# Kernel tuning notes

Hardware: AMD Instinct MI355X
Metric: run time of the kernel (lower is better)

The kernel has to match this reference:

```python
import jax, jax.numpy as jnp
import numpy as np

N = 100000
E = 3200000
D_IN = 128
D_OUT = 64


def setup_inputs() -> dict:
    key = jax.random.key(0)
    k1, k2, k3 = jax.random.split(key, 3)
    x = jax.random.normal(k1, (N, D_IN), dtype=jnp.float32)
    edge_index = jax.random.randint(k2, (2, E), 0, N, dtype=jnp.int64)
    # Glorot-ish init for the GCN weight, zero bias (PyG default has bias)
    W = jax.random.normal(k3, (D_IN, D_OUT), dtype=jnp.float32) * (1.0 / np.sqrt(D_IN))
    b = jnp.zeros((D_OUT,), dtype=jnp.float32)
    return {"x": x, "edge_index": edge_index, "W": W, "b": b}


def gcn_conv(x, edge_index, W, b):
    # PyG GCNConv: add self-loops, symmetric degree normalization,
    # linear transform, then normalized scatter-add aggregation.
    n = x.shape[0]
    self_loops = jnp.arange(n, dtype=edge_index.dtype)
    row = jnp.concatenate([edge_index[0], self_loops])  # targets
    col = jnp.concatenate([edge_index[1], self_loops])  # sources

    ones = jnp.ones_like(row, dtype=x.dtype)
    deg = jax.ops.segment_sum(ones, row, num_segments=n)  # [N]
    deg_inv_sqrt = jnp.where(deg > 0, jax.lax.rsqrt(deg), 0.0)
    norm = deg_inv_sqrt[row] * deg_inv_sqrt[col]  # [E+N]

    h = x @ W  # [N, d_out] -- transform before aggregation (cheap GEMM)
    msgs = norm[:, None] * h[col]  # gather + scale: [E+N, d_out]
    out = jax.ops.segment_sum(msgs, row, num_segments=n)  # scatter-add
    return out + b


def reference(x, edge_index, W, b):
    # CRD.forward: relu(GCNConv(x, edge_index)); dropout is identity in eval.
    return jax.nn.relu(gcn_conv(x, edge_index, W, b))
```

## Files before the change

kernel.cpp:

```cpp
#include <hip/hip_runtime.h>

#define D_IN 128
#define D_OUT 64
#define RSH 7
#define RPS 128
#define NS 1024
#define ACH 5120
#define AREG 10
#define PREG 25
#define CSHIFT 17
#define CMASK 0x1FFFFu

typedef unsigned int u32;
typedef __attribute__((ext_vector_type(8))) short bf16x8;
typedef __attribute__((ext_vector_type(4))) float f32x4;

__device__ inline float u2f(u32 u) {
    union { u32 i; float f; } v; v.i = u; return v.f;
}
__device__ inline unsigned short f2bf(float f) {
    union { float f; u32 i; } v; v.f = f;
    u32 r = v.i + 0x7fffu + ((v.i >> 16) & 1u);
    return (unsigned short)(r >> 16);
}

__global__ __launch_bounds__(256) void k_hist(
    const int* __restrict__ row, u32* __restrict__ stot, int E) {
    __shared__ u32 cnt[NS];
    for (int t = threadIdx.x; t < NS; t += 256) cnt[t] = 0;
    __syncthreads();
    const int stride = gridDim.x * 256;
    for (int e = blockIdx.x * 256 + threadIdx.x; e < E; e += stride)
        atomicAdd(&cnt[(u32)__builtin_nontemporal_load(&row[e]) >> RSH], 1u);
    __syncthreads();
    for (int t = threadIdx.x; t < NS; t += 256) {
        u32 c = cnt[t];
        if (c) atomicAdd(&stot[t], c);
    }
}

__global__ __launch_bounds__(1024) void k_scan1024(
    const u32* __restrict__ stot, u32* __restrict__ sstart,
    u32* __restrict__ gcur, int E) {
    __shared__ u32 tmp[1024];
    const int t = threadIdx.x;
    u32 v = stot[t];
    tmp[t] = v;
    __syncthreads();
    for (int off = 1; off < 1024; off <<= 1) {
        u32 u = (t >= off) ? tmp[t - off] : 0;
        __syncthreads();
        tmp[t] += u;
        __syncthreads();
    }
    u32 ex = tmp[t] - v;
    sstart[t] = ex;
    gcur[t] = ex;
    if (t == 1023) sstart[1024] = (u32)E;
}

__global__ __launch_bounds__(512) void k_part(
    const int* __restrict__ row, const int* __restrict__ col,
    u32* __restrict__ gcur, u32* __restrict__ pk, int E, int CH) {
    __shared__ u32 cnt[NS];
    const int lo = blockIdx.x * CH, hi = min(E, lo + CH);
    const int tid = threadIdx.x;
    u32 rw[PREG], cw[PREG];
#pragma unroll
    for (int k = 0; k < PREG; ++k) {
        int e = lo + tid + k * 512;
        if (e < hi) {
            rw[k] = (u32)__builtin_nontemporal_load(&row[e]);
            cw[k] = (u32)__builtin_nontemporal_load(&col[e]);
        }
    }
    for (int t = tid; t < NS; t += 512) cnt[t] = 0;
    __syncthreads();
#pragma unroll
    for (int k = 0; k < PREG; ++k)
        if (lo + tid + k * 512 < hi) atomicAdd(&cnt[rw[k] >> RSH], 1u);
    __syncthreads();
    for (int t = tid; t < NS; t += 512) {
        u32 c = cnt[t];
        cnt[t] = c ? atomicAdd(&gcur[t], c) : 0u;
    }
    __syncthreads();
#pragma unroll
    for (int k = 0; k < PREG; ++k)
        if (lo + tid + k * 512 < hi) {
            u32 pos = atomicAdd(&cnt[rw[k] >> RSH], 1u);
            pk[pos] = ((rw[k] & (RPS - 1u)) << CSHIFT) | cw[k];
        }
}

__global__ __launch_bounds__(256) void k_deg(
    const u32* __restrict__ pk, const u32* __restrict__ sstart,
    float* __restrict__ dinv, int n) {
    __shared__ u32 cnt[RPS];
    const int s = blockIdx.x, lo = s << RSH;
    if (threadIdx.x < RPS) cnt[threadIdx.x] = 0;
    __syncthreads();
    const u32 beg = sstart[s], end = sstart[s + 1];
    for (u32 i = beg + threadIdx.x; i < end; i += 256)
        atomicAdd(&cnt[pk[i] >> CSHIFT], 1u);
    __syncthreads();
    for (int t = threadIdx.x; t < RPS && lo + t < n; t += 256)
        dinv[lo + t] = rsqrtf((float)(cnt[t] + 1u));
}

__global__ __launch_bounds__(256, 4) void k_gemm(
    const float* __restrict__ x, const float* __restrict__ W,
    const float* __restrict__ dinv, unsigned short* __restrict__ h, int n) {
    __shared__ float Wl[D_IN * D_OUT];
    for (int idx = threadIdx.x; idx < D_IN * D_OUT; idx += 256)
        Wl[idx] = W[idx];
    __syncthreads();

    const int lane = threadIdx.x & 63;
    const int wave = threadIdx.x >> 6;
    const int m = lane & 15, kg = lane >> 4;

    bf16x8 bfr[4][4];
#pragma unroll
    for (int kb = 0; kb < 4; ++kb)
#pragma unroll
        for (int nb = 0; nb < 4; ++nb) {
            bf16x8 f;
#pragma unroll
            for (int j = 0; j < 8; ++j)
                f[j] = (short)f2bf(Wl[(kb * 32 + kg * 8 + j) * D_OUT + nb * 16 + m]);
            bfr[kb][nb] = f;
        }

    const int ntile = (n + 15) >> 4;
    for (int tile = blockIdx.x * 4 + wave; tile < ntile; tile += gridDim.x * 4) {
        const int i0 = tile << 4;
        const int arow = min(i0 + m, n - 1);
        const float* xr = &x[(size_t)arow * D_IN + kg * 8];

        f32x4 acc[4];
#pragma unroll
        for (int nb = 0; nb < 4; ++nb) acc[nb] = (f32x4){0.f, 0.f, 0.f, 0.f};

#pragma unroll
        for (int kb = 0; kb < 4; ++kb) {
            float4 xa = *(const float4*)(xr + kb * 32);
            float4 xb = *(const float4*)(xr + kb * 32 + 4);
            bf16x8 af;
            af[0] = (short)f2bf(xa.x); af[1] = (short)f2bf(xa.y);
            af[2] = (short)f2bf(xa.z); af[3] = (short)f2bf(xa.w);
            af[4] = (short)f2bf(xb.x); af[5] = (short)f2bf(xb.y);
            af[6] = (short)f2bf(xb.z); af[7] = (short)f2bf(xb.w);
#pragma unroll
            for (int nb = 0; nb < 4; ++nb)
                acc[nb] = __builtin_amdgcn_mfma_f32_16x16x32_bf16(
                    af, bfr[kb][nb], acc[nb], 0, 0, 0);
        }
#pragma unroll
        for (int i = 0; i < 4; ++i) {
            int r = i0 + kg * 4 + i;
            if (r < n) {
                float d = dinv[r];
#pragma unroll
                for (int nb = 0; nb < 4; ++nb)
                    h[(size_t)r * D_OUT + nb * 16 + m] = f2bf(d * acc[nb][i]);
            }
        }
    }
}

__global__ __launch_bounds__(512, 4) void k_aggr(
    const unsigned short* __restrict__ h, const u32* __restrict__ pk,
    const u32* __restrict__ sstart, const float* __restrict__ dinv,
    const float* __restrict__ bias, float* __restrict__ out, int n) {
    __shared__ u32 cnt[RPS], eptr[RPS], cur[RPS];
    __shared__ u32 cols[ACH];
    const int s = blockIdx.x, lo = s << RSH;
    const int rows = min(RPS, n - lo);
    const int tid = threadIdx.x;
    const int wave = tid >> 6, lane = tid & 63;
    const int qd = lane >> 4, l15 = lane & 15;
    const uint2* hp2 = (const uint2*)h;

    float a0[16], a1[16], a2[16], a3[16];
#pragma unroll
    for (int k = 0; k < 16; ++k) { a0[k] = 0.f; a1[k] = 0.f; a2[k] = 0.f; a3[k] = 0.f; }

    const u32 beg = sstart[s], end = sstart[s + 1];
    for (u32 cb = beg; cb < end; cb += ACH) {
        const u32 ce = min(end, cb + (u32)ACH);
        const int m = (int)(ce - cb);
        u32 w[AREG];
#pragma unroll
        for (int k = 0; k < AREG; ++k) {
            int i = tid + k * 512;
            if (i < m) w[k] = __builtin_nontemporal_load(&pk[cb + i]);
        }
        if (tid < RPS) cnt[tid] = 0;
        __syncthreads();
#pragma unroll
        for (int k = 0; k < AREG; ++k)
            if (tid + k * 512 < m) atomicAdd(&cnt[w[k] >> CSHIFT], 1u);
        __syncthreads();
        if (tid < 64) {
            u32 c0 = cnt[2 * tid], c1 = cnt[2 * tid + 1];
            u32 sv = c0 + c1;
#pragma unroll
            for (int d = 1; d < 64; d <<= 1) {
                u32 t = __shfl_up(sv, d);
                if (tid >= d) sv += t;
            }
            u32 ex = sv - (c0 + c1);
            eptr[2 * tid] = ex;          cur[2 * tid] = ex;
            eptr[2 * tid + 1] = ex + c0; cur[2 * tid + 1] = ex + c0;
        }
        __syncthreads();
#pragma unroll
        for (int k = 0; k < AREG; ++k)
            if (tid + k * 512 < m) {
                u32 pos = atomicAdd(&cur[w[k] >> CSHIFT], 1u);
                cols[pos] = w[k] & CMASK;
            }
        __syncthreads();
#pragma unroll
        for (int k = 0; k < 16; ++k) {
            int q = wave + 8 * k;
            if (q < rows) {
                const int b1 = (int)eptr[q] + (int)cnt[q];
                int t = (int)eptr[q];
                for (; t + 32 <= b1; t += 32) {
                    u32 c[8]; uint2 u[8];
#pragma unroll
                    for (int j = 0; j < 8; ++j) c[j] = cols[t + 4 * j + qd];
#pragma unroll
                    for (int j = 0; j < 8; ++j) u[j] = hp2[(size_t)c[j] * 16 + l15];
#pragma unroll
                    for (int j = 0; j < 8; ++j) {
                        a0[k] += u2f(u[j].x << 16); a1[k] += u2f(u[j].x & 0xffff0000u);
                        a2[k] += u2f(u[j].y << 16); a3[k] += u2f(u[j].y & 0xffff0000u);
                    }
                }
                for (; t + 16 <= b1; t += 16) {
                    u32 c[4]; uint2 u[4];
#pragma unroll
                    for (int j = 0; j < 4; ++j) c[j] = cols[t + 4 * j + qd];
#pragma unroll
                    for (int j = 0; j < 4; ++j) u[j] = hp2[(size_t)c[j] * 16 + l15];
#pragma unroll
                    for (int j = 0; j < 4; ++j) {
                        a0[k] += u2f(u[j].x << 16); a1[k] += u2f(u[j].x & 0xffff0000u);
                        a2[k] += u2f(u[j].y << 16); a3[k] += u2f(u[j].y & 0xffff0000u);
                    }
                }
                for (; t + 4 <= b1; t += 4) {
                    u32 c = cols[t + qd];
                    uint2 u = hp2[(size_t)c * 16 + l15];
                    a0[k] += u2f(u.x << 16); a1[k] += u2f(u.x & 0xffff0000u);
                    a2[k] += u2f(u.y << 16); a3[k] += u2f(u.y & 0xffff0000u);
                }
                const int rem = b1 - t;
                if (qd < rem) {
                    u32 c = cols[t + qd];
                    uint2 u = hp2[(size_t)c * 16 + l15];
                    a0[k] += u2f(u.x << 16); a1[k] += u2f(u.x & 0xffff0000u);
                    a2[k] += u2f(u.y << 16); a3[k] += u2f(u.y & 0xffff0000u);
                }
            }
        }
        __syncthreads();
    }
#pragma unroll
    for (int k = 0; k < 16; ++k) {
        int q = wave + 8 * k;
        if (q >= rows) continue;
        float r0 = a0[k], r1 = a1[k], r2 = a2[k], r3 = a3[k];
        r0 += __shfl_xor(r0, 16); r0 += __shfl_xor(r0, 32);
        r1 += __shfl_xor(r1, 16); r1 += __shfl_xor(r1, 32);
        r2 += __shfl_xor(r2, 16); r2 += __shfl_xor(r2, 32);
        r3 += __shfl_xor(r3, 16); r3 += __shfl_xor(r3, 32);
        int i = lo + q;
        uint2 us = hp2[(size_t)i * 16 + l15];
        r0 += u2f(us.x << 16); r1 += u2f(us.x & 0xffff0000u);
        r2 += u2f(us.y << 16); r3 += u2f(us.y & 0xffff0000u);
        float d = dinv[i];
        float4 bb = *(const float4*)&bias[l15 * 4];
        float4 o;
        o.x = fmaxf(fmaf(d, r0, bb.x), 0.f);
        o.y = fmaxf(fmaf(d, r1, bb.y), 0.f);
        o.z = fmaxf(fmaf(d, r2, bb.z), 0.f);
        o.w = fmaxf(fmaf(d, r3, bb.w), 0.f);
        if (qd == 0)
            *(float4*)&out[(size_t)i * D_OUT + l15 * 4] = o;
    }
}

extern "C" void kernel_launch(void* const* d_in, const int* in_sizes, int n_in,
                              void* d_out, int out_size, void* d_ws, size_t ws_size,
                              hipStream_t stream) {
    const float* x  = (const float*)d_in[0];
    const int*   ei = (const int*)d_in[1];
    const float* W  = (const float*)d_in[2];
    const float* b  = (const float*)d_in[3];
    const int n = in_sizes[0] / D_IN;
    const int E = in_sizes[1] / 2;
    const int* row = ei;
    const int* col = ei + E;

    char* basep = (char*)d_ws;
    size_t off = 0;
    auto alloc = [&](size_t bytes) { char* p = basep + off; off += (bytes + 63) & ~(size_t)63; return p; };
    unsigned short* h      = (unsigned short*)alloc((size_t)n * D_OUT * 2);
    u32*            pk     = (u32*)alloc((size_t)E * 4);
    float*          dinv   = (float*)alloc((size_t)n * 4);
    u32*            stot   = (u32*)alloc((size_t)NS * 4);
    u32*            sstart = (u32*)alloc((size_t)(NS + 1) * 4);
    u32*            gcur   = (u32*)alloc((size_t)NS * 4);

    const int NSL = (n + RPS - 1) / RPS;
    const int NPB = 256;
    const int CH  = (E + NPB - 1) / NPB;

    hipMemsetAsync(stot, 0, (size_t)NS * 4, stream);
    k_hist<<<1024, 256, 0, stream>>>(row, stot, E);
    k_scan1024<<<1, 1024, 0, stream>>>(stot, sstart, gcur, E);
    k_part<<<NPB, 512, 0, stream>>>(row, col, gcur, pk, E, CH);
    k_deg<<<NSL, 256, 0, stream>>>(pk, sstart, dinv, n);
    k_gemm<<<1024, 256, 0, stream>>>(x, W, dinv, h, n);
    k_aggr<<<NSL, 512, 0, stream>>>(h, pk, sstart, dinv, b, (float*)d_out, n);
}
```

Measured before the change: 170.0 us.

## Split bf16 features into two 32-column halves and aggregate in two gather passes

The GEMM now writes the transformed features as two separate bf16 arrays, each holding 32 columns per node. The aggregation kernel gathers each half in its own pass over the edge chunk, with one 32-bit load per lane instead of a 64-bit load. The aim is to halve the table each pass touches so the random neighbour gathers hit cache more often. In exchange, every edge index is read from shared memory twice, loop overhead doubles, each gather moves narrower segments, and the 16-edge unrolled tail path is dropped.

```diff
diff --git a/kernel.cpp b/kernel.cpp
--- a/kernel.cpp
+++ b/kernel.cpp
@@ -110,7 +110,8 @@
 
 __global__ __launch_bounds__(256, 4) void k_gemm(
     const float* __restrict__ x, const float* __restrict__ W,
-    const float* __restrict__ dinv, unsigned short* __restrict__ h, int n) {
+    const float* __restrict__ dinv, unsigned short* __restrict__ h0,
+    unsigned short* __restrict__ h1, int n) {
     __shared__ float Wl[D_IN * D_OUT];
     for (int idx = threadIdx.x; idx < D_IN * D_OUT; idx += 256)
         Wl[idx] = W[idx];
@@ -161,18 +162,51 @@
             int r = i0 + kg * 4 + i;
             if (r < n) {
                 float d = dinv[r];
-#pragma unroll
-                for (int nb = 0; nb < 4; ++nb)
-                    h[(size_t)r * D_OUT + nb * 16 + m] = f2bf(d * acc[nb][i]);
+                h0[(size_t)r * 32 + m]      = f2bf(d * acc[0][i]);
+                h0[(size_t)r * 32 + 16 + m] = f2bf(d * acc[1][i]);
+                h1[(size_t)r * 32 + m]      = f2bf(d * acc[2][i]);
+                h1[(size_t)r * 32 + 16 + m] = f2bf(d * acc[3][i]);
             }
         }
     }
 }
 
+#define GATHER_PASS(HP, A0, A1)                                              \
+    for (int k = 0; k < 16; ++k) {                                           \
+        int q = wave + 8 * k;                                                \
+        if (q < rows) {                                                      \
+            const int b1 = (int)eptr[q] + (int)cnt[q];                       \
+            int t = (int)eptr[q];                                            \
+            for (; t + 32 <= b1; t += 32) {                                  \
+                u32 c[8], u[8];                                              \
+                _Pragma("unroll")                                            \
+                for (int j = 0; j < 8; ++j) c[j] = cols[t + 4 * j + qd];     \
+                _Pragma("unroll")                                            \
+                for (int j = 0; j < 8; ++j) u[j] = HP[(size_t)c[j] * 16 + l15]; \
+                _Pragma("unroll")                                            \
+                for (int j = 0; j < 8; ++j) {                                \
+                    A0[k] += u2f(u[j] << 16); A1[k] += u2f(u[j] & 0xffff0000u); \
+                }                                                            \
+            }                                                                \
+            for (; t + 4 <= b1; t += 4) {                                    \
+                u32 c = cols[t + qd];                                        \
+                u32 u = HP[(size_t)c * 16 + l15];                            \
+                A0[k] += u2f(u << 16); A1[k] += u2f(u & 0xffff0000u);        \
+            }                                                                \
+            const int rem = b1 - t;                                          \
+            if (qd < rem) {                                                  \
+                u32 c = cols[t + qd];                                        \
+                u32 u = HP[(size_t)c * 16 + l15];                            \
+                A0[k] += u2f(u << 16); A1[k] += u2f(u & 0xffff0000u);        \
+            }                                                                \
+        }                                                                    \
+    }
+
 __global__ __launch_bounds__(512, 4) void k_aggr(
-    const unsigned short* __restrict__ h, const u32* __restrict__ pk,
-    const u32* __restrict__ sstart, const float* __restrict__ dinv,
-    const float* __restrict__ bias, float* __restrict__ out, int n) {
+    const unsigned short* __restrict__ h0, const unsigned short* __restrict__ h1,
+    const u32* __restrict__ pk, const u32* __restrict__ sstart,
+    const float* __restrict__ dinv, const float* __restrict__ bias,
+    float* __restrict__ out, int n) {
     __shared__ u32 cnt[RPS], eptr[RPS], cur[RPS];
     __shared__ u32 cols[ACH];
     const int s = blockIdx.x, lo = s << RSH;
@@ -180,7 +214,8 @@
     const int tid = threadIdx.x;
     const int wave = tid >> 6, lane = tid & 63;
     const int qd = lane >> 4, l15 = lane & 15;
-    const uint2* hp2 = (const uint2*)h;
+    const u32* hp0 = (const u32*)h0;
+    const u32* hp1 = (const u32*)h1;
 
     float a0[16], a1[16], a2[16], a3[16];
 #pragma unroll
@@ -223,74 +258,37 @@
             }
         __syncthreads();
 #pragma unroll
-        for (int k = 0; k < 16; ++k) {
-            int q = wave + 8 * k;
-            if (q < rows) {
-                const int b1 = (int)eptr[q] + (int)cnt[q];
-                int t = (int)eptr[q];
-                for (; t + 32 <= b1; t += 32) {
-                    u32 c[8]; uint2 u[8];
-#pragma unroll
-                    for (int j = 0; j < 8; ++j) c[j] = cols[t + 4 * j + qd];
-#pragma unroll
-                    for (int j = 0; j < 8; ++j) u[j] = hp2[(size_t)c[j] * 16 + l15];
-#pragma unroll
-                    for (int j = 0; j < 8; ++j) {
-                        a0[k] += u2f(u[j].x << 16); a1[k] += u2f(u[j].x & 0xffff0000u);
-                        a2[k] += u2f(u[j].y << 16); a3[k] += u2f(u[j].y & 0xffff0000u);
-                    }
-                }
-                for (; t + 16 <= b1; t += 16) {
-                    u32 c[4]; uint2 u[4];
-#pragma unroll
-                    for (int j = 0; j < 4; ++j) c[j] = cols[t + 4 * j + qd];
-#pragma unroll
-                    for (int j = 0; j < 4; ++j) u[j] = hp2[(size_t)c[j] * 16 + l15];
-#pragma unroll
-                    for (int j = 0; j < 4; ++j) {
-                        a0[k] += u2f(u[j].x << 16); a1[k] += u2f(u[j].x & 0xffff0000u);
-                        a2[k] += u2f(u[j].y << 16); a3[k] += u2f(u[j].y & 0xffff0000u);
-                    }
-                }
-                for (; t + 4 <= b1; t += 4) {
-                    u32 c = cols[t + qd];
-                    uint2 u = hp2[(size_t)c * 16 + l15];
-                    a0[k] += u2f(u.x << 16); a1[k] += u2f(u.x & 0xffff0000u);
-                    a2[k] += u2f(u.y << 16); a3[k] += u2f(u.y & 0xffff0000u);
-                }
-                const int rem = b1 - t;
-                if (qd < rem) {
-                    u32 c = cols[t + qd];
-                    uint2 u = hp2[(size_t)c * 16 + l15];
-                    a0[k] += u2f(u.x << 16); a1[k] += u2f(u.x & 0xffff0000u);
-                    a2[k] += u2f(u.y << 16); a3[k] += u2f(u.y & 0xffff0000u);
-                }
-            }
-        }
+        GATHER_PASS(hp0, a0, a1)
+#pragma unroll
+        GATHER_PASS(hp1, a2, a3)
         __syncthreads();
     }
 #pragma unroll
     for (int k = 0; k < 16; ++k) {
         int q = wave + 8 * k;
         if (q >= rows) continue;
+        int i = lo + q;
+        float d = dinv[i];
         float r0 = a0[k], r1 = a1[k], r2 = a2[k], r3 = a3[k];
         r0 += __shfl_xor(r0, 16); r0 += __shfl_xor(r0, 32);
         r1 += __shfl_xor(r1, 16); r1 += __shfl_xor(r1, 32);
         r2 += __shfl_xor(r2, 16); r2 += __shfl_xor(r2, 32);
         r3 += __shfl_xor(r3, 16); r3 += __shfl_xor(r3, 32);
-        int i = lo + q;
-        uint2 us = hp2[(size_t)i * 16 + l15];
-        r0 += u2f(us.x << 16); r1 += u2f(us.x & 0xffff0000u);
-        r2 += u2f(us.y << 16); r3 += u2f(us.y & 0xffff0000u);
-        float d = dinv[i];
-        float4 bb = *(const float4*)&bias[l15 * 4];
-        float4 o;
-        o.x = fmaxf(fmaf(d, r0, bb.x), 0.f);
-        o.y = fmaxf(fmaf(d, r1, bb.y), 0.f);
-        o.z = fmaxf(fmaf(d, r2, bb.z), 0.f);
-        o.w = fmaxf(fmaf(d, r3, bb.w), 0.f);
-        if (qd == 0)
-            *(float4*)&out[(size_t)i * D_OUT + l15 * 4] = o;
+        u32 us0 = hp0[(size_t)i * 16 + l15];
+        u32 us1 = hp1[(size_t)i * 16 + l15];
+        r0 += u2f(us0 << 16); r1 += u2f(us0 & 0xffff0000u);
+        r2 += u2f(us1 << 16); r3 += u2f(us1 & 0xffff0000u);
+        if (qd == 0) {
+            float2 b0 = *(const float2*)&bias[2 * l15];
+            float2 b1 = *(const float2*)&bias[32 + 2 * l15];
+            float2 o0, o1;
+            o0.x = fmaxf(fmaf(d, r0, b0.x), 0.f);
+            o0.y = fmaxf(fmaf(d, r1, b0.y), 0.f);
+            o1.x = fmaxf(fmaf(d, r2, b1.x), 0.f);
+            o1.y = fmaxf(fmaf(d, r3, b1.y), 0.f);
+            *(float2*)&out[(size_t)i * D_OUT + 2 * l15] = o0;
+            *(float2*)&out[(size_t)i * D_OUT + 32 + 2 * l15] = o1;
+        }
     }
 }
 
@@ -309,7 +307,8 @@
     char* basep = (char*)d_ws;
     size_t off = 0;
     auto alloc = [&](size_t bytes) { char* p = basep + off; off += (bytes + 63) & ~(size_t)63; return p; };
-    unsigned short* h      = (unsigned short*)alloc((size_t)n * D_OUT * 2);
+    unsigned short* h0     = (unsigned short*)alloc((size_t)n * 32 * 2);
+    unsigned short* h1     = (unsigned short*)alloc((size_t)n * 32 * 2);
     u32*            pk     = (u32*)alloc((size_t)E * 4);
     float*          dinv   = (float*)alloc((size_t)n * 4);
     u32*            stot   = (u32*)alloc((size_t)NS * 4);
@@ -325,6 +324,6 @@
     k_scan1024<<<1, 1024, 0, stream>>>(stot, sstart, gcur, E);
     k_part<<<NPB, 512, 0, stream>>>(row, col, gcur, pk, E, CH);
     k_deg<<<NSL, 256, 0, stream>>>(pk, sstart, dinv, n);
-    k_gemm<<<1024, 256, 0, stream>>>(x, W, dinv, h, n);
-    k_aggr<<<NSL, 512, 0, stream>>>(h, pk, sstart, dinv, b, (float*)d_out, n);
-}
+    k_gemm<<<1024, 256, 0, stream>>>(x, W, dinv, h0, h1, n);
+    k_aggr<<<NSL, 512, 0, stream>>>(h0, h1, pk, sstart, dinv, b, (float*)d_out, n);
+}
```

New measurement: 248.9 us. +46.4%, slower.
